# Kernel optimization log

Measured on AMD Instinct MI355X. Metric: run time of the kernel, lower is better.

The kernel has to match this reference:

```python
import jax, jax.numpy as jnp
import numpy as np

B, S, D, H = 2, 2048, 1024, 16
HD = D // H
EPS = 1e-5


def setup_inputs() -> dict:
    key = jax.random.key(0)
    ks = jax.random.split(key, 12)
    n = lambda k, shp, s=0.02: jax.random.normal(k, shp, dtype=jnp.float32) * s
    return {
        "x": jax.random.normal(ks[0], (B, S, D), dtype=jnp.float32),
        "Wq": n(ks[1], (D, D)), "bq": jnp.zeros((D,), jnp.float32),
        "Wk": n(ks[2], (D, D)), "bk": jnp.zeros((D,), jnp.float32),
        "Wv": n(ks[3], (D, D)), "bv": jnp.zeros((D,), jnp.float32),
        "Wo": n(ks[4], (D, D)), "bo": jnp.zeros((D,), jnp.float32),
        "rel_bias": n(ks[5], (H, S, S)),  # relative_position_bias param (window==S)
        "gamma": jnp.ones((D,), jnp.float32),
        "beta": jnp.zeros((D,), jnp.float32),
    }


def reference(x, Wq, bq, Wk, bk, Wv, bv, Wo, bo, rel_bias, gamma, beta):
    b, s, d = x.shape
    # projections (torch Linear: x @ W.T + b), split heads -> (b, h, s, hd)
    def proj(W, bias):
        return (x @ W.T + bias).reshape(b, s, H, HD).transpose(0, 2, 1, 3)
    Q, K, V = proj(Wq, bq), proj(Wk, bk), proj(Wv, bv)

    scores = jnp.einsum("bhqd,bhkd->bhqk", Q, K) / jnp.sqrt(jnp.float32(HD))
    # additive causal mask (-inf strictly above diagonal) + relative position bias
    i = jnp.arange(s)
    causal = jnp.where(i[:, None] >= i[None, :], 0.0, -jnp.inf).astype(scores.dtype)
    scores = scores + causal[None, None] + rel_bias[None, :, :s, :s]

    attn = jax.nn.softmax(scores, axis=-1)  # dropout is identity in eval mode
    attended = jnp.einsum("bhqk,bhkd->bhqd", attn, V)
    attended = attended.transpose(0, 2, 1, 3).reshape(b, s, d)

    out = attended @ Wo.T + bo
    # residual + LayerNorm(eps=1e-5)
    y = out + x
    mu = jnp.mean(y, axis=-1, keepdims=True)
    var = jnp.var(y, axis=-1, keepdims=True)
    return (y - mu) / jnp.sqrt(var + EPS) * gamma + beta
```

## Files before the change

### kernel.cpp

```cpp
#include <hip/hip_runtime.h>

typedef __attribute__((ext_vector_type(8))) short short8;
typedef __attribute__((ext_vector_type(4))) float f32x4;
typedef unsigned short u16;
typedef __attribute__((ext_vector_type(4))) unsigned short u16x4;

#define S_LEN 2048
#define DMODEL 1024
#define NH 16
#define HD 64

static __device__ __forceinline__ u16 f2bf(float f) {
    union { float f; unsigned u; } x; x.f = f;
    unsigned r = x.u + 0x7fffu + ((x.u >> 16) & 1u);
    return (u16)(r >> 16);
}

static __device__ __forceinline__ unsigned cvtpk_bf16(float lo, float hi) {
    unsigned r;
    asm("v_cvt_pk_bf16_f32 %0, %1, %2" : "=v"(r) : "v"(lo), "v"(hi));
    return r;
}

#define GLD_LDS16(g, l) __builtin_amdgcn_global_load_lds( \
    (const __attribute__((address_space(1))) void*)(g),   \
    (__attribute__((address_space(3))) void*)(l), 16, 0, 0)

#define MFMA16(a, b, c) __builtin_amdgcn_mfma_f32_16x16x32_bf16(a, b, c, 0, 0, 0)

#define LOAD_FENCE() asm volatile("" ::: "memory")

#define TILE_SYNC() do {                                          \
    asm volatile("s_waitcnt vmcnt(4)" ::: "memory");              \
    __builtin_amdgcn_s_barrier();                                 \
    __builtin_amdgcn_sched_barrier(0);                            \
} while (0)

#define TILE_SYNC_FULL() do {                                     \
    asm volatile("s_waitcnt vmcnt(0)" ::: "memory");              \
    __builtin_amdgcn_s_barrier();                                 \
    __builtin_amdgcn_sched_barrier(0);                            \
} while (0)

__global__ __launch_bounds__(256) void cast_kernel(const float* __restrict__ in,
                                                   u16* __restrict__ out, int n4) {
    int i = blockIdx.x * 256 + threadIdx.x;
    if (i < n4) {
        const float4 v = reinterpret_cast<const float4*>(in)[i];
        u16x4 o;
        o.x = f2bf(v.x); o.y = f2bf(v.y); o.z = f2bf(v.z); o.w = f2bf(v.w);
        reinterpret_cast<u16x4*>(out)[i] = o;
    }
}

__global__ __launch_bounds__(256) void cast4_kernel(
    const float* __restrict__ w0, const float* __restrict__ w1,
    const float* __restrict__ w2, const float* __restrict__ w3,
    u16* __restrict__ o0, u16* __restrict__ o1,
    u16* __restrict__ o2, u16* __restrict__ o3, int n4) {
    const int z = blockIdx.y;
    const float* in = (z == 0) ? w0 : (z == 1) ? w1 : (z == 2) ? w2 : w3;
    u16* out = (z == 0) ? o0 : (z == 1) ? o1 : (z == 2) ? o2 : o3;
    int i = blockIdx.x * 256 + threadIdx.x;
    if (i < n4) {
        const float4 v = reinterpret_cast<const float4*>(in)[i];
        u16x4 o;
        o.x = f2bf(v.x); o.y = f2bf(v.y); o.z = f2bf(v.z); o.w = f2bf(v.w);
        reinterpret_cast<u16x4*>(out)[i] = o;
    }
}

__global__ __launch_bounds__(256) void gemm_qkv_kernel(
    const u16* __restrict__ xbf,
    const u16* __restrict__ wqbf, const u16* __restrict__ wkbf, const u16* __restrict__ wvbf,
    const float* __restrict__ bq, const float* __restrict__ bk, const float* __restrict__ bv,
    u16* __restrict__ qout, u16* __restrict__ kout, u16* __restrict__ vtout)
{
    __shared__ u16 As[128][64];
    __shared__ u16 Bs[128][64];

    const int z = blockIdx.z;
    const u16* __restrict__ W = (z == 0) ? wqbf : (z == 1) ? wkbf : wvbf;
    const float* __restrict__ bias = (z == 0) ? bq : (z == 1) ? bk : bv;

    const int tid  = threadIdx.x;
    const int lane = tid & 63;
    const int wid  = tid >> 6;
    const int wm = (wid >> 1) * 64;
    const int wn = (wid & 1) * 64;
    const int lr = lane & 15;
    const int lg = lane >> 4;

    const int m0 = blockIdx.y * 128;
    const int n0 = blockIdx.x * 128;

    f32x4 acc[4][4] = {};

    for (int kt = 0; kt < DMODEL; kt += 64) {
#pragma unroll
        for (int i = 0; i < 4; ++i) {
            const int c = i * 256 + tid;
            const int row = c >> 3;
            const int kk = (c & 7) * 8;
            GLD_LDS16(xbf + (size_t)(m0 + row) * DMODEL + kt + kk, &As[0][0] + c * 8);
        }
#pragma unroll
        for (int i = 0; i < 4; ++i) {
            const int c = i * 256 + tid;
            const int row = c >> 3;
            const int kk = (c & 7) * 8;
            GLD_LDS16(W + (size_t)(n0 + row) * DMODEL + kt + kk, &Bs[0][0] + c * 8);
        }
        __syncthreads();
#pragma unroll
        for (int ks = 0; ks < 2; ++ks) {
            short8 af[4], bfr[4];
#pragma unroll
            for (int t = 0; t < 4; ++t)
                af[t] = *(const short8*)&As[wm + t * 16 + lr][ks * 32 + lg * 8];
#pragma unroll
            for (int t = 0; t < 4; ++t)
                bfr[t] = *(const short8*)&Bs[wn + t * 16 + lr][ks * 32 + lg * 8];
#pragma unroll
            for (int mt = 0; mt < 4; ++mt)
#pragma unroll
                for (int nt = 0; nt < 4; ++nt)
                    acc[mt][nt] = MFMA16(af[mt], bfr[nt], acc[mt][nt]);
        }
        __syncthreads();
    }

#pragma unroll
    for (int mt = 0; mt < 4; ++mt) {
#pragma unroll
        for (int nt = 0; nt < 4; ++nt) {
            const int n = n0 + wn + nt * 16 + lr;
            const int h = (n >> 6) & (NH - 1);
            const int hd = n & (HD - 1);
            const float bia = bias[n];
#pragma unroll
            for (int r = 0; r < 4; ++r) {
                const int m = m0 + wm + mt * 16 + lg * 4 + r;
                const int bb = m >> 11;
                const int ss = m & (S_LEN - 1);
                const float v = acc[mt][nt][r] + bia;
                const int bh = bb * NH + h;
                if (z == 0) {
                    qout[((size_t)bh * S_LEN + ss) * HD + hd] = f2bf(v * 0.125f);
                } else if (z == 1) {
                    kout[((size_t)bh * S_LEN + ss) * HD + hd] = f2bf(v);
                } else {
                    vtout[((size_t)bh * HD + hd) * S_LEN + ss] = f2bf(v);
                }
            }
        }
    }
}

__global__ __launch_bounds__(256, 3) void attn_kernel(
    const u16* __restrict__ qbf, const u16* __restrict__ kbf,
    const u16* __restrict__ vtbf, const float* __restrict__ rel,
    u16* __restrict__ att)
{
    __shared__ u16 Klds[2][64][64];
    __shared__ u16 Vlds[2][64][64];
    __shared__ u16 P[4][16][72];

    const int tid  = threadIdx.x;
    const int lane = tid & 63;
    const int wid  = tid >> 6;
    const int c = lane & 15;
    const int g = lane >> 4;

    const int h = blockIdx.x >> 1;
    const int b = blockIdx.x & 1;
    const int bh = b * NH + h;
    const int blkq = gridDim.y - 1 - blockIdx.y;
    const int q0 = blkq * 64;
    const int qv = q0 + wid * 16 + c;

    const size_t base = (size_t)bh * S_LEN * HD;

    const short8 qf0 = *(const short8*)&qbf[base + (size_t)qv * HD + g * 8];
    const short8 qf1 = *(const short8*)&qbf[base + (size_t)qv * HD + 32 + g * 8];

    const float* __restrict__ relrow = rel + (size_t)h * S_LEN * S_LEN + (size_t)qv * S_LEN;

    f32x4 o[4] = {};
    float m_run = -3e38f, l_run = 0.f;
    f32x4 rbA[4], rbB[4];

    const int nkt = blkq + 1;

    auto stage = [&](int kt, int bb) {
        const int k0 = kt * 64;
#pragma unroll
        for (int i = 0; i < 2; ++i) {
            const int s = i * 256 + tid;
            const int row = s >> 3;
            const int u = (s & 7) ^ (row & 7);
            GLD_LDS16(kbf + base + (size_t)(k0 + row) * HD + u * 8,
                      &Klds[bb][0][0] + s * 8);
        }
#pragma unroll
        for (int i = 0; i < 2; ++i) {
            const int s = i * 256 + tid;
            const int row = s >> 3;
            const int u = (s & 7) ^ (row & 7);
            GLD_LDS16(vtbf + base + (size_t)row * S_LEN + k0 + u * 8,
                      &Vlds[bb][0][0] + s * 8);
        }
    };

    auto rel_into = [&](f32x4 (&rb)[4], int kt) {
        const float* rn = relrow + kt * 64;
        rb[0] = *(const f32x4*)&rn[g * 4];
        rb[1] = *(const f32x4*)&rn[16 + g * 4];
        rb[2] = *(const f32x4*)&rn[32 + g * 4];
        rb[3] = *(const f32x4*)&rn[48 + g * 4];
    };

    auto compute_tile = [&](int cur, int k0, bool diag, const f32x4 (&rb)[4]) {
        short8 kf[8];
#pragma unroll
        for (int mt = 0; mt < 4; ++mt) {
            const u16* kp = &Klds[cur][0][0] + (mt * 16 + c) * 64;
            kf[2 * mt]     = *(const short8*)(kp + ((g ^ (c & 7)) * 8));
            kf[2 * mt + 1] = *(const short8*)(kp + (((4 + g) ^ (c & 7)) * 8));
        }
        f32x4 st[4] = {};
        __builtin_amdgcn_s_setprio(1);
#pragma unroll
        for (int mt = 0; mt < 4; ++mt) {
            st[mt] = MFMA16(kf[2 * mt], qf0, st[mt]);
            st[mt] = MFMA16(kf[2 * mt + 1], qf1, st[mt]);
        }
        __builtin_amdgcn_s_setprio(0);

        short8 vf[8];
#pragma unroll
        for (int nt = 0; nt < 4; ++nt) {
            const u16* vp = &Vlds[cur][0][0] + (nt * 16 + c) * 64;
            vf[2 * nt]     = *(const short8*)(vp + ((g ^ (c & 7)) * 8));
            vf[2 * nt + 1] = *(const short8*)(vp + (((4 + g) ^ (c & 7)) * 8));
        }

        float tm = -3e38f;
        if (diag) {
#pragma unroll
            for (int mt = 0; mt < 4; ++mt)
#pragma unroll
                for (int r = 0; r < 4; ++r) {
                    const int k = k0 + mt * 16 + g * 4 + r;
                    float sv = st[mt][r] + rb[mt][r];
                    if (k > qv) sv = -1e30f;
                    st[mt][r] = sv;
                    tm = fmaxf(tm, sv);
                }
        } else {
#pragma unroll
            for (int mt = 0; mt < 4; ++mt)
#pragma unroll
                for (int r = 0; r < 4; ++r) {
                    const float sv = st[mt][r] + rb[mt][r];
                    st[mt][r] = sv;
                    tm = fmaxf(tm, sv);
                }
        }

        if (!__all(tm <= m_run + 8.0f)) {
            tm = fmaxf(tm, __shfl_xor(tm, 16));
            tm = fmaxf(tm, __shfl_xor(tm, 32));
            const float mn = fmaxf(m_run, tm);
            const float sc = __expf(m_run - mn);
            m_run = mn;
            l_run *= sc;
#pragma unroll
            for (int r = 0; r < 4; ++r) {
                const float scq = __shfl(sc, g * 4 + r);
#pragma unroll
                for (int nt = 0; nt < 4; ++nt) o[nt][r] *= scq;
            }
        }

        float rsum = 0.f;
#pragma unroll
        for (int mt = 0; mt < 4; ++mt)
#pragma unroll
            for (int r = 0; r < 4; ++r) {
                const float e = __expf(st[mt][r] - m_run);
                st[mt][r] = e;
                rsum += e;
            }
        rsum += __shfl_xor(rsum, 16);
        rsum += __shfl_xor(rsum, 32);
        l_run += rsum;

#pragma unroll
        for (int mt = 0; mt < 4; ++mt) {
            uint2 pk;
            pk.x = cvtpk_bf16(st[mt][0], st[mt][1]);
            pk.y = cvtpk_bf16(st[mt][2], st[mt][3]);
            *(uint2*)&P[wid][c][mt * 16 + g * 4] = pk;
        }
        const short8 pa0 = *(const short8*)&P[wid][c][g * 8];
        const short8 pa1 = *(const short8*)&P[wid][c][32 + g * 8];

        __builtin_amdgcn_s_setprio(1);
        o[0] = MFMA16(pa0, vf[0], o[0]);
        o[0] = MFMA16(pa1, vf[1], o[0]);
        o[1] = MFMA16(pa0, vf[2], o[1]);
        o[1] = MFMA16(pa1, vf[3], o[1]);
        o[2] = MFMA16(pa0, vf[4], o[2]);
        o[2] = MFMA16(pa1, vf[5], o[2]);
        o[3] = MFMA16(pa0, vf[6], o[3]);
        o[3] = MFMA16(pa1, vf[7], o[3]);
        __builtin_amdgcn_s_setprio(0);
    };

    stage(0, 0);
    LOAD_FENCE();
    rel_into(rbA, 0);
    if (nkt > 1) rel_into(rbB, 1);
    __syncthreads();

    int cur = 0;
    int t = 0;
    while (t + 1 < nkt - 1) {
        stage(t + 1, cur ^ 1);
        LOAD_FENCE();
        compute_tile(cur, t * 64, false, rbA);
        rel_into(rbA, t + 2);
        LOAD_FENCE();
        TILE_SYNC();
        cur ^= 1;

        stage(t + 2, cur ^ 1);
        LOAD_FENCE();
        compute_tile(cur, (t + 1) * 64, false, rbB);
        if (t + 3 < nkt) {
            rel_into(rbB, t + 3);
            LOAD_FENCE();
            TILE_SYNC();
        } else {
            LOAD_FENCE();
            TILE_SYNC_FULL();
        }
        cur ^= 1;

        t += 2;
    }

    if (t < nkt - 1) {
        stage(t + 1, cur ^ 1);
        LOAD_FENCE();
        compute_tile(cur, t * 64, false, rbA);
        TILE_SYNC_FULL();
        cur ^= 1;
        compute_tile(cur, (nkt - 1) * 64, true, rbB);
    } else {
        compute_tile(cur, (nkt - 1) * 64, true, rbA);
    }

#pragma unroll
    for (int r = 0; r < 4; ++r) {
        const float linv = 1.0f / __shfl(l_run, g * 4 + r);
        const int q = q0 + wid * 16 + g * 4 + r;
#pragma unroll
        for (int nt = 0; nt < 4; ++nt) {
            att[((size_t)(b * S_LEN + q)) * DMODEL + h * HD + nt * 16 + c] =
                f2bf(o[nt][r] * linv);
        }
    }
}

__global__ __launch_bounds__(256) void gemm_o_kernel(
    const u16* __restrict__ att, const u16* __restrict__ wobf,
    const float* __restrict__ bo, const float* __restrict__ x,
    float* __restrict__ y)
{
    __shared__ u16 As[128][64];
    __shared__ u16 Bs[128][64];

    const int tid  = threadIdx.x;
    const int lane = tid & 63;
    const int wid  = tid >> 6;
    const int wm = (wid >> 1) * 64;
    const int wn = (wid & 1) * 64;
    const int lr = lane & 15;
    const int lg = lane >> 4;

    const int m0 = blockIdx.y * 128;
    const int n0 = blockIdx.x * 128;

    f32x4 acc[4][4] = {};

    for (int kt = 0; kt < DMODEL; kt += 64) {
#pragma unroll
        for (int i = 0; i < 4; ++i) {
            const int c = i * 256 + tid;
            const int row = c >> 3;
            const int kk = (c & 7) * 8;
            GLD_LDS16(att + (size_t)(m0 + row) * DMODEL + kt + kk, &As[0][0] + c * 8);
        }
#pragma unroll
        for (int i = 0; i < 4; ++i) {
            const int c = i * 256 + tid;
            const int row = c >> 3;
            const int kk = (c & 7) * 8;
            GLD_LDS16(wobf + (size_t)(n0 + row) * DMODEL + kt + kk, &Bs[0][0] + c * 8);
        }
        __syncthreads();
#pragma unroll
        for (int ks = 0; ks < 2; ++ks) {
            short8 af[4], bfr[4];
#pragma unroll
            for (int t = 0; t < 4; ++t)
                af[t] = *(const short8*)&As[wm + t * 16 + lr][ks * 32 + lg * 8];
#pragma unroll
            for (int t = 0; t < 4; ++t)
                bfr[t] = *(const short8*)&Bs[wn + t * 16 + lr][ks * 32 + lg * 8];
#pragma unroll
            for (int mt = 0; mt < 4; ++mt)
#pragma unroll
                for (int nt = 0; nt < 4; ++nt)
                    acc[mt][nt] = MFMA16(af[mt], bfr[nt], acc[mt][nt]);
        }
        __syncthreads();
    }

#pragma unroll
    for (int mt = 0; mt < 4; ++mt) {
#pragma unroll
        for (int nt = 0; nt < 4; ++nt) {
            const int n = n0 + wn + nt * 16 + lr;
            const float bia = bo[n];
#pragma unroll
            for (int r = 0; r < 4; ++r) {
                const int m = m0 + wm + mt * 16 + lg * 4 + r;
                const size_t idx = (size_t)m * DMODEL + n;
                y[idx] = acc[mt][nt][r] + bia + x[idx];
            }
        }
    }
}

__global__ __launch_bounds__(256) void ln_kernel(
    const float* __restrict__ y, const float* __restrict__ gamma,
    const float* __restrict__ beta, float* __restrict__ out)
{
    __shared__ float red[8];
    const int row = blockIdx.x;
    const int tid = threadIdx.x;
    const size_t base = (size_t)row * DMODEL + tid * 4;
    const float4 v = *(const float4*)&y[base];
    float s  = v.x + v.y + v.z + v.w;
    float ss = v.x * v.x + v.y * v.y + v.z * v.z + v.w * v.w;
#pragma unroll
    for (int off = 1; off < 64; off <<= 1) {
        s  += __shfl_xor(s, off);
        ss += __shfl_xor(ss, off);
    }
    const int w = tid >> 6;
    if ((tid & 63) == 0) { red[w] = s; red[4 + w] = ss; }
    __syncthreads();
    s  = red[0] + red[1] + red[2] + red[3];
    ss = red[4] + red[5] + red[6] + red[7];
    const float mu = s * (1.0f / DMODEL);
    const float var = ss * (1.0f / DMODEL) - mu * mu;
    const float rstd = rsqrtf(var + 1e-5f);
    const int col = tid * 4;
    float4 o;
    o.x = (v.x - mu) * rstd * gamma[col + 0] + beta[col + 0];
    o.y = (v.y - mu) * rstd * gamma[col + 1] + beta[col + 1];
    o.z = (v.z - mu) * rstd * gamma[col + 2] + beta[col + 2];
    o.w = (v.w - mu) * rstd * gamma[col + 3] + beta[col + 3];
    *(float4*)&out[base] = o;
}

extern "C" void kernel_launch(void* const* d_in, const int* in_sizes, int n_in,
                              void* d_out, int out_size, void* d_ws, size_t ws_size,
                              hipStream_t stream) {
    (void)in_sizes; (void)n_in; (void)out_size; (void)ws_size;
    const float* x     = (const float*)d_in[0];
    const float* Wq    = (const float*)d_in[1];
    const float* bq    = (const float*)d_in[2];
    const float* Wk    = (const float*)d_in[3];
    const float* bk    = (const float*)d_in[4];
    const float* Wv    = (const float*)d_in[5];
    const float* bv    = (const float*)d_in[6];
    const float* Wo    = (const float*)d_in[7];
    const float* bo    = (const float*)d_in[8];
    const float* rel   = (const float*)d_in[9];
    const float* gamma = (const float*)d_in[10];
    const float* beta  = (const float*)d_in[11];
    float* out = (float*)d_out;

    char* ws = (char*)d_ws;
    u16* xbf   = (u16*)(ws);
    u16* wqbf  = (u16*)(ws + ( 8u << 20));
    u16* wkbf  = (u16*)(ws + (10u << 20));
    u16* wvbf  = (u16*)(ws + (12u << 20));
    u16* wobf  = (u16*)(ws + (14u << 20));
    u16* qbf   = (u16*)(ws + (16u << 20));
    u16* kbf   = (u16*)(ws + (24u << 20));
    u16* vtbf  = (u16*)(ws + (32u << 20));
    u16* attbf = (u16*)(ws + (40u << 20));
    float* y   = (float*)(ws + (48u << 20));

    cast_kernel<<<4096, 256, 0, stream>>>(x, xbf, (2 * S_LEN * DMODEL) / 4);
    cast4_kernel<<<dim3(1024, 4), 256, 0, stream>>>(
        Wq, Wk, Wv, Wo, wqbf, wkbf, wvbf, wobf, (DMODEL * DMODEL) / 4);

    gemm_qkv_kernel<<<dim3(8, 32, 3), 256, 0, stream>>>(
        xbf, wqbf, wkbf, wvbf, bq, bk, bv, qbf, kbf, vtbf);

    attn_kernel<<<dim3(2 * NH, 32), 256, 0, stream>>>(qbf, kbf, vtbf, rel, attbf);

    gemm_o_kernel<<<dim3(8, 32), 256, 0, stream>>>(attbf, wobf, bo, x, y);

    ln_kernel<<<2 * S_LEN, 256, 0, stream>>>(y, gamma, beta, out);
}
```

Baseline: 175.4 us.

## Double-buffer QKV and output GEMM LDS tiles with XOR-swizzled layout

Both projection GEMMs now use two LDS buffers with a K-step of 32, prefetching the next tile via global_load_lds while MFMAs run on the current one. The old version loaded and synced once per 64-wide step. An XOR swizzle on 16-byte chunks is added to the LDS layout to reduce bank conflicts on fragment reads. The cost is twice as many K iterations and barriers, plus reliance on the LOAD_FENCE/TILE_SYNC_FULL macros for correct ordering.

```diff
diff --git a/kernel.cpp b/kernel.cpp
--- a/kernel.cpp
+++ b/kernel.cpp
@@ -70,14 +70,31 @@
     }
 }
 
+
+#define GEMM_STAGE(SRC, SRCLD, KCOL, LDSBASE) do {                            \
+    _Pragma("unroll")                                                          \
+    for (int _i = 0; _i < 2; ++_i) {                                           \
+        const int _s = _i * 256 + tid;                                         \
+        const int _row = _s >> 2;                                              \
+        const int _u = (_s & 3) ^ ((_row >> 1) & 3);                           \
+        GLD_LDS16((SRC) + (size_t)(_row) * (SRCLD) + (KCOL) + _u * 8,          \
+                  (LDSBASE) + _s * 8);                                         \
+    }                                                                          \
+} while (0)
+
+static __device__ __forceinline__ short8 lds_frag(const u16* base, int row, int lg) {
+    const int u = lg ^ ((row >> 1) & 3);
+    return *(const short8*)(base + row * 32 + u * 8);
+}
+
 __global__ __launch_bounds__(256) void gemm_qkv_kernel(
     const u16* __restrict__ xbf,
     const u16* __restrict__ wqbf, const u16* __restrict__ wkbf, const u16* __restrict__ wvbf,
     const float* __restrict__ bq, const float* __restrict__ bk, const float* __restrict__ bv,
     u16* __restrict__ qout, u16* __restrict__ kout, u16* __restrict__ vtout)
 {
-    __shared__ u16 As[128][64];
-    __shared__ u16 Bs[128][64];
+    __shared__ u16 As[2][128][32];
+    __shared__ u16 Bs[2][128][32];
 
     const int z = blockIdx.z;
     const u16* __restrict__ W = (z == 0) ? wqbf : (z == 1) ? wkbf : wvbf;
@@ -94,41 +111,47 @@
     const int m0 = blockIdx.y * 128;
     const int n0 = blockIdx.x * 128;
 
+    const u16* __restrict__ Abase = xbf + (size_t)m0 * DMODEL;
+    const u16* __restrict__ Bbase = W + (size_t)n0 * DMODEL;
+
     f32x4 acc[4][4] = {};
 
-    for (int kt = 0; kt < DMODEL; kt += 64) {
-#pragma unroll
-        for (int i = 0; i < 4; ++i) {
-            const int c = i * 256 + tid;
-            const int row = c >> 3;
-            const int kk = (c & 7) * 8;
-            GLD_LDS16(xbf + (size_t)(m0 + row) * DMODEL + kt + kk, &As[0][0] + c * 8);
-        }
-#pragma unroll
-        for (int i = 0; i < 4; ++i) {
-            const int c = i * 256 + tid;
-            const int row = c >> 3;
-            const int kk = (c & 7) * 8;
-            GLD_LDS16(W + (size_t)(n0 + row) * DMODEL + kt + kk, &Bs[0][0] + c * 8);
-        }
-        __syncthreads();
-#pragma unroll
-        for (int ks = 0; ks < 2; ++ks) {
-            short8 af[4], bfr[4];
-#pragma unroll
-            for (int t = 0; t < 4; ++t)
-                af[t] = *(const short8*)&As[wm + t * 16 + lr][ks * 32 + lg * 8];
-#pragma unroll
-            for (int t = 0; t < 4; ++t)
-                bfr[t] = *(const short8*)&Bs[wn + t * 16 + lr][ks * 32 + lg * 8];
-#pragma unroll
-            for (int mt = 0; mt < 4; ++mt)
-#pragma unroll
-                for (int nt = 0; nt < 4; ++nt)
-                    acc[mt][nt] = MFMA16(af[mt], bfr[nt], acc[mt][nt]);
-        }
-        __syncthreads();
-    }
+#define QKV_COMPUTE(BUF)                                                      \
+    do {                                                                      \
+        short8 af[4], bfr[4];                                                 \
+        _Pragma("unroll")                                                     \
+        for (int t = 0; t < 4; ++t)                                           \
+            af[t] = lds_frag(&As[BUF][0][0], wm + t * 16 + lr, lg);           \
+        _Pragma("unroll")                                                     \
+        for (int t = 0; t < 4; ++t)                                           \
+            bfr[t] = lds_frag(&Bs[BUF][0][0], wn + t * 16 + lr, lg);          \
+        _Pragma("unroll")                                                     \
+        for (int mt = 0; mt < 4; ++mt)                                        \
+            _Pragma("unroll")                                                 \
+            for (int nt = 0; nt < 4; ++nt)                                    \
+                acc[mt][nt] = MFMA16(af[mt], bfr[nt], acc[mt][nt]);           \
+    } while (0)
+
+    GEMM_STAGE(Abase, DMODEL, 0, &As[0][0][0]);
+    GEMM_STAGE(Bbase, DMODEL, 0, &Bs[0][0][0]);
+    __syncthreads();
+
+    for (int kt = 0; kt < 32; kt += 2) {
+        GEMM_STAGE(Abase, DMODEL, (kt + 1) * 32, &As[1][0][0]);
+        GEMM_STAGE(Bbase, DMODEL, (kt + 1) * 32, &Bs[1][0][0]);
+        LOAD_FENCE();
+        QKV_COMPUTE(0);
+        TILE_SYNC_FULL();
+
+        if (kt + 2 < 32) {
+            GEMM_STAGE(Abase, DMODEL, (kt + 2) * 32, &As[0][0][0]);
+            GEMM_STAGE(Bbase, DMODEL, (kt + 2) * 32, &Bs[0][0][0]);
+            LOAD_FENCE();
+        }
+        QKV_COMPUTE(1);
+        TILE_SYNC_FULL();
+    }
+#undef QKV_COMPUTE
 
 #pragma unroll
     for (int mt = 0; mt < 4; ++mt) {
@@ -379,8 +402,8 @@
     const float* __restrict__ bo, const float* __restrict__ x,
     float* __restrict__ y)
 {
-    __shared__ u16 As[128][64];
-    __shared__ u16 Bs[128][64];
+    __shared__ u16 As[2][128][32];
+    __shared__ u16 Bs[2][128][32];
 
     const int tid  = threadIdx.x;
     const int lane = tid & 63;
@@ -393,41 +416,47 @@
     const int m0 = blockIdx.y * 128;
     const int n0 = blockIdx.x * 128;
 
+    const u16* __restrict__ Abase = att + (size_t)m0 * DMODEL;
+    const u16* __restrict__ Bbase = wobf + (size_t)n0 * DMODEL;
+
     f32x4 acc[4][4] = {};
 
-    for (int kt = 0; kt < DMODEL; kt += 64) {
-#pragma unroll
-        for (int i = 0; i < 4; ++i) {
-            const int c = i * 256 + tid;
-            const int row = c >> 3;
-            const int kk = (c & 7) * 8;
-            GLD_LDS16(att + (size_t)(m0 + row) * DMODEL + kt + kk, &As[0][0] + c * 8);
-        }
-#pragma unroll
-        for (int i = 0; i < 4; ++i) {
-            const int c = i * 256 + tid;
-            const int row = c >> 3;
-            const int kk = (c & 7) * 8;
-            GLD_LDS16(wobf + (size_t)(n0 + row) * DMODEL + kt + kk, &Bs[0][0] + c * 8);
-        }
-        __syncthreads();
-#pragma unroll
-        for (int ks = 0; ks < 2; ++ks) {
-            short8 af[4], bfr[4];
-#pragma unroll
-            for (int t = 0; t < 4; ++t)
-                af[t] = *(const short8*)&As[wm + t * 16 + lr][ks * 32 + lg * 8];
-#pragma unroll
-            for (int t = 0; t < 4; ++t)
-                bfr[t] = *(const short8*)&Bs[wn + t * 16 + lr][ks * 32 + lg * 8];
-#pragma unroll
-            for (int mt = 0; mt < 4; ++mt)
-#pragma unroll
-                for (int nt = 0; nt < 4; ++nt)
-                    acc[mt][nt] = MFMA16(af[mt], bfr[nt], acc[mt][nt]);
-        }
-        __syncthreads();
-    }
+#define O_COMPUTE(BUF)                                                        \
+    do {                                                                      \
+        short8 af[4], bfr[4];                                                 \
+        _Pragma("unroll")                                                     \
+        for (int t = 0; t < 4; ++t)                                           \
+            af[t] = lds_frag(&As[BUF][0][0], wm + t * 16 + lr, lg);           \
+        _Pragma("unroll")                                                     \
+        for (int t = 0; t < 4; ++t)                                           \
+            bfr[t] = lds_frag(&Bs[BUF][0][0], wn + t * 16 + lr, lg);          \
+        _Pragma("unroll")                                                     \
+        for (int mt = 0; mt < 4; ++mt)                                        \
+            _Pragma("unroll")                                                 \
+            for (int nt = 0; nt < 4; ++nt)                                    \
+                acc[mt][nt] = MFMA16(af[mt], bfr[nt], acc[mt][nt]);           \
+    } while (0)
+
+    GEMM_STAGE(Abase, DMODEL, 0, &As[0][0][0]);
+    GEMM_STAGE(Bbase, DMODEL, 0, &Bs[0][0][0]);
+    __syncthreads();
+
+    for (int kt = 0; kt < 32; kt += 2) {
+        GEMM_STAGE(Abase, DMODEL, (kt + 1) * 32, &As[1][0][0]);
+        GEMM_STAGE(Bbase, DMODEL, (kt + 1) * 32, &Bs[1][0][0]);
+        LOAD_FENCE();
+        O_COMPUTE(0);
+        TILE_SYNC_FULL();
+
+        if (kt + 2 < 32) {
+            GEMM_STAGE(Abase, DMODEL, (kt + 2) * 32, &As[0][0][0]);
+            GEMM_STAGE(Bbase, DMODEL, (kt + 2) * 32, &Bs[0][0][0]);
+            LOAD_FENCE();
+        }
+        O_COMPUTE(1);
+        TILE_SYNC_FULL();
+    }
+#undef O_COMPUTE
 
 #pragma unroll
     for (int mt = 0; mt < 4; ++mt) {
```

Result: no change. 172.1 us (-1.9%).
